# Optimization experiments

Measured on AMD Instinct MI355X. Metric: run time of the kernel, lower is better.

## Reference

```python
import jax, jax.numpy as jnp
import numpy as np

H = 32          # hidden_size
L = 10          # linear_size
EPS = 1e-14


def _lstm_cell(x, h, c, Wih, Whh, bih, bhh):
    # torch LSTMCell: gates ordered [i, f, g, o]
    gates = x @ Wih.T + bih + h @ Whh.T + bhh
    i, f, g, o = jnp.split(gates, 4, axis=-1)
    i = jax.nn.sigmoid(i)
    f = jax.nn.sigmoid(f)
    g = jnp.tanh(g)
    o = jax.nn.sigmoid(o)
    c_new = f * c + i * g
    h_new = o * jnp.tanh(c_new)
    return h_new, c_new


def setup_inputs() -> dict:
    key = jax.random.key(0)
    ks = jax.random.split(key, 24)
    B, N = 8, 100000
    inp = {
        "x": jax.random.normal(ks[0], (B, N), jnp.float32),
        "grad": jax.random.normal(ks[1], (B, N), jnp.float32),
        "h0": jax.random.normal(ks[2], (B, N, H), jnp.float32),
        "c0": jax.random.normal(ks[3], (B, N, H), jnp.float32),
        "h1": jax.random.normal(ks[4], (B, N, H), jnp.float32),
        "c1": jax.random.normal(ks[5], (B, N, H), jnp.float32),
        # initial_transform: Linear(2, L) -> tanh -> Linear(L, L)
        "W1": jax.random.normal(ks[6], (L, 2), jnp.float32) * 0.3,
        "b1": jax.random.normal(ks[7], (L,), jnp.float32) * 0.1,
        "W2": jax.random.normal(ks[8], (L, L), jnp.float32) * 0.3,
        "b2": jax.random.normal(ks[9], (L,), jnp.float32) * 0.1,
        # LSTMCell layer 0 (input L) and layer 1 (input H)
        "Wih0": jax.random.normal(ks[10], (4 * H, L), jnp.float32) * 0.1,
        "Whh0": jax.random.normal(ks[11], (4 * H, H), jnp.float32) * 0.1,
        "bih0": jax.random.normal(ks[12], (4 * H,), jnp.float32) * 0.1,
        "bhh0": jax.random.normal(ks[13], (4 * H,), jnp.float32) * 0.1,
        "Wih1": jax.random.normal(ks[14], (4 * H, H), jnp.float32) * 0.1,
        "Whh1": jax.random.normal(ks[15], (4 * H, H), jnp.float32) * 0.1,
        "bih1": jax.random.normal(ks[16], (4 * H,), jnp.float32) * 0.1,
        "bhh1": jax.random.normal(ks[17], (4 * H,), jnp.float32) * 0.1,
        # fc: Linear(H, 1)
        "Wfc": jax.random.normal(ks[18], (1, H), jnp.float32) * 0.1,
        "bfc": jax.random.normal(ks[19], (1,), jnp.float32) * 0.1,
    }
    return inp


def reference(x, grad, h0, c0, h1, c1, W1, b1, W2, b2,
              Wih0, Whh0, bih0, bhh0, Wih1, Whh1, bih1, bhh1, Wfc, bfc):
    B, N = x.shape
    BN = B * N
    g = grad.reshape(BN, 1)
    # gradient preprocessing: [sign, log(|g| + eps)]
    inp = jnp.concatenate([jnp.sign(g), jnp.log(jnp.abs(g) + EPS)], axis=1)  # (BN, 2)
    t = jnp.tanh(inp @ W1.T + b1) @ W2.T + b2                                # (BN, L)
    # batched across all n variables simultaneously (no cross-variable recurrence)
    h0n, c0n = _lstm_cell(t, h0.reshape(BN, H), c0.reshape(BN, H), Wih0, Whh0, bih0, bhh0)
    h1n, c1n = _lstm_cell(h0n, h1.reshape(BN, H), c1.reshape(BN, H), Wih1, Whh1, bih1, bhh1)
    delta = (h1n @ Wfc.T + bfc).reshape(B, N)
    x_new = x + delta
    return (x_new,
            h0n.reshape(B, N, H), c0n.reshape(B, N, H),
            h1n.reshape(B, N, H), c1n.reshape(B, N, H),
            delta)
```

## Files before the change

kernel.cpp:

```cpp
#include <hip/hip_runtime.h>


typedef __attribute__((ext_vector_type(8))) short bf16x8;
typedef __attribute__((ext_vector_type(4))) float f32x4;

#define HH 32
#define LL 10
#define NG 128
#define NW 8
#define BLK 512
#define TP 36

__device__ __forceinline__ short f2bf(float x) {
  __bf16 b = (__bf16)x;
  return __builtin_bit_cast(short, b);
}
__device__ __forceinline__ float fsig(float x) {
  return __builtin_amdgcn_rcpf(1.0f + __expf(-x));
}
__device__ __forceinline__ float ftanh(float x) {
  return fmaf(2.0f, __builtin_amdgcn_rcpf(1.0f + __expf(-2.0f * x)), -1.0f);
}
#define LDS_FENCE() asm volatile("s_waitcnt lgkmcnt(0)" ::: "memory")

#define LOADT(P, STV) do {                                                   \
    const size_t ro_ = (size_t)(ebase + (STV) * 16 + col) * HH + 8 * g;      \
    P##hv0 = reinterpret_cast<const float4*>(h0 + ro_)[0];                   \
    P##hv1 = reinterpret_cast<const float4*>(h0 + ro_)[1];                   \
    P##cv0 = reinterpret_cast<const float4*>(c0 + ro_)[0];                   \
    P##cv1 = reinterpret_cast<const float4*>(c0 + ro_)[1];                   \
    P##wv0 = reinterpret_cast<const float4*>(h1 + ro_)[0];                   \
    P##wv1 = reinterpret_cast<const float4*>(h1 + ro_)[1];                   \
    P##dv0 = reinterpret_cast<const float4*>(c1 + ro_)[0];                   \
    P##dv1 = reinterpret_cast<const float4*>(c1 + ro_)[1];                   \
  } while (0)

#define COMPUTE(P, STV) do {                                                  \
    const int m16_ = ebase + (STV) * 16;                                      \
    const size_t rowoff_ = (size_t)(m16_ + col) * HH + 8 * g;                 \
    bf16x8 a_t = {0, 0, 0, 0, 0, 0, 0, 0};                                    \
    if (g == 0) a_t = *reinterpret_cast<const bf16x8*>(&tsg0[w][(STV) * 16 + col][0]); \
    else if (g == 1) {                                                        \
      a_t[0] = tsg1[w][(STV) * 16 + col][0];                                  \
      a_t[1] = tsg1[w][(STV) * 16 + col][1];                                  \
    }                                                                         \
    bf16x8 a_h0;                                                              \
    a_h0[0] = f2bf(P##hv0.x); a_h0[1] = f2bf(P##hv0.y);                       \
    a_h0[2] = f2bf(P##hv0.z); a_h0[3] = f2bf(P##hv0.w);                       \
    a_h0[4] = f2bf(P##hv1.x); a_h0[5] = f2bf(P##hv1.y);                       \
    a_h0[6] = f2bf(P##hv1.z); a_h0[7] = f2bf(P##hv1.w);                       \
    f32x4 acc[8];                                                             \
    _Pragma("unroll")                                                         \
    for (int nt = 0; nt < 8; ++nt) {                                          \
      float bv = biasv0[nt];                                                  \
      f32x4 a = {bv, bv, bv, bv};                                             \
      acc[nt] = a;                                                            \
    }                                                                         \
    _Pragma("unroll")                                                         \
    for (int nt = 0; nt < 8; ++nt) {                                          \
      bf16x8 bih = {0, 0, 0, 0, 0, 0, 0, 0};                                  \
      if (g < 2) bih = *reinterpret_cast<const bf16x8*>(&wih0L[g][nt * 16 + col][0]); \
      acc[nt] = __builtin_amdgcn_mfma_f32_16x16x32_bf16(a_t, bih, acc[nt], 0, 0, 0);  \
      bf16x8 bhh = *reinterpret_cast<const bf16x8*>(&whh0L[g][nt * 16 + col][0]);     \
      acc[nt] = __builtin_amdgcn_mfma_f32_16x16x32_bf16(a_h0, bhh, acc[nt], 0, 0, 0); \
    }                                                                         \
    *reinterpret_cast<float4*>(&tbuf[w][col][8 * g])     = P##cv0;            \
    *reinterpret_cast<float4*>(&tbuf[w][col][8 * g + 4]) = P##cv1;            \
    LDS_FENCE();                                                              \
    float c0r[2][4];                                                          \
    _Pragma("unroll")                                                         \
    for (int kk = 0; kk < 2; ++kk)                                            \
      _Pragma("unroll")                                                       \
      for (int r = 0; r < 4; ++r)                                             \
        c0r[kk][r] = tbuf[w][mrow + r][16 * kk + col];                        \
    LDS_FENCE();                                                              \
    float hnv[2][4], cnv[2][4];                                               \
    _Pragma("unroll")                                                         \
    for (int kk = 0; kk < 2; ++kk)                                            \
      _Pragma("unroll")                                                       \
      for (int r = 0; r < 4; ++r) {                                           \
        float iv = fsig(acc[0 + kk][r]);                                      \
        float fv = fsig(acc[2 + kk][r]);                                      \
        float gv = ftanh(acc[4 + kk][r]);                                     \
        float ov = fsig(acc[6 + kk][r]);                                      \
        float cn = fv * c0r[kk][r] + iv * gv;                                 \
        float hn = ov * ftanh(cn);                                            \
        cnv[kk][r] = cn;                                                      \
        hnv[kk][r] = hn;                                                      \
      }                                                                       \
    _Pragma("unroll")                                                         \
    for (int kk = 0; kk < 2; ++kk)                                            \
      _Pragma("unroll")                                                       \
      for (int r = 0; r < 4; ++r)                                             \
        tbuf[w][mrow + r][16 * kk + col] = hnv[kk][r];                        \
    LDS_FENCE();                                                              \
    float4 hnr0 = *reinterpret_cast<const float4*>(&tbuf[w][col][8 * g]);     \
    float4 hnr1 = *reinterpret_cast<const float4*>(&tbuf[w][col][8 * g + 4]); \
    LDS_FENCE();                                                              \
    *reinterpret_cast<float4*>(h0out + rowoff_)     = hnr0;                   \
    *reinterpret_cast<float4*>(h0out + rowoff_ + 4) = hnr1;                   \
    bf16x8 a_hn;                                                              \
    a_hn[0] = f2bf(hnr0.x); a_hn[1] = f2bf(hnr0.y);                           \
    a_hn[2] = f2bf(hnr0.z); a_hn[3] = f2bf(hnr0.w);                           \
    a_hn[4] = f2bf(hnr1.x); a_hn[5] = f2bf(hnr1.y);                           \
    a_hn[6] = f2bf(hnr1.z); a_hn[7] = f2bf(hnr1.w);                           \
    _Pragma("unroll")                                                         \
    for (int kk = 0; kk < 2; ++kk)                                            \
      _Pragma("unroll")                                                       \
      for (int r = 0; r < 4; ++r)                                             \
        tbuf[w][mrow + r][16 * kk + col] = cnv[kk][r];                        \
    LDS_FENCE();                                                              \
    float4 cnr0 = *reinterpret_cast<const float4*>(&tbuf[w][col][8 * g]);     \
    float4 cnr1 = *reinterpret_cast<const float4*>(&tbuf[w][col][8 * g + 4]); \
    LDS_FENCE();                                                              \
    *reinterpret_cast<float4*>(c0out + rowoff_)     = cnr0;                   \
    *reinterpret_cast<float4*>(c0out + rowoff_ + 4) = cnr1;                   \
    *reinterpret_cast<float4*>(&tbuf[w][col][8 * g])     = P##dv0;            \
    *reinterpret_cast<float4*>(&tbuf[w][col][8 * g + 4]) = P##dv1;            \
    LDS_FENCE();                                                              \
    float c1r[2][4];                                                          \
    _Pragma("unroll")                                                         \
    for (int kk = 0; kk < 2; ++kk)                                            \
      _Pragma("unroll")                                                       \
      for (int r = 0; r < 4; ++r)                                             \
        c1r[kk][r] = tbuf[w][mrow + r][16 * kk + col];                        \
    LDS_FENCE();                                                              \
    bf16x8 a_h1;                                                              \
    a_h1[0] = f2bf(P##wv0.x); a_h1[1] = f2bf(P##wv0.y);                       \
    a_h1[2] = f2bf(P##wv0.z); a_h1[3] = f2bf(P##wv0.w);                       \
    a_h1[4] = f2bf(P##wv1.x); a_h1[5] = f2bf(P##wv1.y);                       \
    a_h1[6] = f2bf(P##wv1.z); a_h1[7] = f2bf(P##wv1.w);                       \
    _Pragma("unroll")                                                         \
    for (int nt = 0; nt < 8; ++nt) {                                          \
      float bv = biasv1[nt];                                                  \
      f32x4 a = {bv, bv, bv, bv};                                             \
      acc[nt] = a;                                                            \
    }                                                                         \
    _Pragma("unroll")                                                         \
    for (int nt = 0; nt < 8; ++nt) {                                          \
      bf16x8 bih = *reinterpret_cast<const bf16x8*>(&wih1L[g][nt * 16 + col][0]);     \
      acc[nt] = __builtin_amdgcn_mfma_f32_16x16x32_bf16(a_hn, bih, acc[nt], 0, 0, 0); \
      bf16x8 bhh = *reinterpret_cast<const bf16x8*>(&whh1L[g][nt * 16 + col][0]);     \
      acc[nt] = __builtin_amdgcn_mfma_f32_16x16x32_bf16(a_h1, bhh, acc[nt], 0, 0, 0); \
    }                                                                         \
    float dsum[4] = {0.f, 0.f, 0.f, 0.f};                                     \
    _Pragma("unroll")                                                         \
    for (int kk = 0; kk < 2; ++kk) {                                          \
      const float wf = kk ? wfc1 : wfc0;                                      \
      _Pragma("unroll")                                                       \
      for (int r = 0; r < 4; ++r) {                                           \
        float iv = fsig(acc[0 + kk][r]);                                      \
        float fv = fsig(acc[2 + kk][r]);                                      \
        float gv = ftanh(acc[4 + kk][r]);                                     \
        float ov = fsig(acc[6 + kk][r]);                                      \
        float cn = fv * c1r[kk][r] + iv * gv;                                 \
        float hn = ov * ftanh(cn);                                            \
        cnv[kk][r] = cn;                                                      \
        hnv[kk][r] = hn;                                                      \
        dsum[r] += hn * wf;                                                   \
      }                                                                       \
    }                                                                         \
    _Pragma("unroll")                                                         \
    for (int kk = 0; kk < 2; ++kk)                                            \
      _Pragma("unroll")                                                       \
      for (int r = 0; r < 4; ++r)                                             \
        tbuf[w][mrow + r][16 * kk + col] = hnv[kk][r];                        \
    LDS_FENCE();                                                              \
    float4 h1r0 = *reinterpret_cast<const float4*>(&tbuf[w][col][8 * g]);     \
    float4 h1r1 = *reinterpret_cast<const float4*>(&tbuf[w][col][8 * g + 4]); \
    LDS_FENCE();                                                              \
    *reinterpret_cast<float4*>(h1out + rowoff_)     = h1r0;                   \
    *reinterpret_cast<float4*>(h1out + rowoff_ + 4) = h1r1;                   \
    _Pragma("unroll")                                                         \
    for (int kk = 0; kk < 2; ++kk)                                            \
      _Pragma("unroll")                                                       \
      for (int r = 0; r < 4; ++r)                                             \
        tbuf[w][mrow + r][16 * kk + col] = cnv[kk][r];                        \
    LDS_FENCE();                                                              \
    float4 c1r0 = *reinterpret_cast<const float4*>(&tbuf[w][col][8 * g]);     \
    float4 c1r1 = *reinterpret_cast<const float4*>(&tbuf[w][col][8 * g + 4]); \
    LDS_FENCE();                                                              \
    *reinterpret_cast<float4*>(c1out + rowoff_)     = c1r0;                   \
    *reinterpret_cast<float4*>(c1out + rowoff_ + 4) = c1r1;                   \
    _Pragma("unroll")                                                         \
    for (int off = 1; off < 16; off <<= 1) {                                  \
      _Pragma("unroll")                                                       \
      for (int r = 0; r < 4; ++r) dsum[r] += __shfl_xor(dsum[r], off, 64);    \
    }                                                                         \
    if (col == 0) {                                                           \
      const int e4 = m16_ + mrow;                                             \
      float4 xv = *reinterpret_cast<const float4*>(x + e4);                   \
      float4 dv = {dsum[0] + bfcv, dsum[1] + bfcv, dsum[2] + bfcv, dsum[3] + bfcv}; \
      *reinterpret_cast<float4*>(dout + e4) = dv;                             \
      float4 xn = {xv.x + dv.x, xv.y + dv.y, xv.z + dv.z, xv.w + dv.w};       \
      *reinterpret_cast<float4*>(xout + e4) = xn;                             \
    }                                                                         \
  } while (0)

__global__ __launch_bounds__(BLK, 2) void l2o_fused(
    const float* __restrict__ x, const float* __restrict__ grad,
    const float* __restrict__ h0, const float* __restrict__ c0,
    const float* __restrict__ h1, const float* __restrict__ c1,
    const float* __restrict__ W1, const float* __restrict__ b1,
    const float* __restrict__ W2, const float* __restrict__ b2,
    const float* __restrict__ Wih0, const float* __restrict__ Whh0,
    const float* __restrict__ bih0, const float* __restrict__ bhh0,
    const float* __restrict__ Wih1, const float* __restrict__ Whh1,
    const float* __restrict__ bih1, const float* __restrict__ bhh1,
    const float* __restrict__ Wfc, const float* __restrict__ bfc,
    float* __restrict__ out, int BNi)
{
  const size_t BN = (size_t)BNi;
  float* __restrict__ xout  = out;
  float* __restrict__ h0out = out + BN;
  float* __restrict__ c0out = out + BN + BN * HH;
  float* __restrict__ h1out = out + BN + 2 * BN * HH;
  float* __restrict__ c1out = out + BN + 3 * BN * HH;
  float* __restrict__ dout  = out + BN + 4 * BN * HH;

  __shared__ __align__(16) short wih0L[2][NG][8];
  __shared__ __align__(16) short whh0L[4][NG][8];
  __shared__ __align__(16) short wih1L[4][NG][8];
  __shared__ __align__(16) short whh1L[4][NG][8];
  __shared__ __align__(16) short tsg0[NW][64][8];
  __shared__ __align__(4)  short tsg1[NW][64][2];
  __shared__ __align__(16) float tbuf[NW][16][TP];

  const int tid = threadIdx.x;
  const int lane = tid & 63;
  const int w = tid >> 6;
  const int col = lane & 15;
  const int g = lane >> 4;
  const int mrow = 4 * g;

  const int ebase = blockIdx.x * (NW * 64) + w * 64;
  const bool active = ebase < BNi;

  float4 Ahv0, Ahv1, Acv0, Acv1, Awv0, Awv1, Adv0, Adv1;
  float4 Bhv0, Bhv1, Bcv0, Bcv1, Bwv0, Bwv1, Bdv0, Bdv1;

  if (active) LOADT(A, 0);

  for (int idx = tid; idx < NG * HH; idx += BLK) {
    int n = idx >> 5, k = idx & 31;
    whh0L[k >> 3][n][k & 7] = f2bf(Whh0[n * HH + k]);
    wih1L[k >> 3][n][k & 7] = f2bf(Wih1[n * HH + k]);
    whh1L[k >> 3][n][k & 7] = f2bf(Whh1[n * HH + k]);
  }
  for (int idx = tid; idx < NG * 16; idx += BLK) {
    int n = idx >> 4, k = idx & 15;
    wih0L[k >> 3][n][k & 7] = (k < LL) ? f2bf(Wih0[n * LL + k]) : (short)0;
  }

  float biasv0[8], biasv1[8];
#pragma unroll
  for (int nt = 0; nt < 8; ++nt) {
    biasv0[nt] = bih0[nt * 16 + col] + bhh0[nt * 16 + col];
    biasv1[nt] = bih1[nt * 16 + col] + bhh1[nt * 16 + col];
  }
  const float wfc0 = Wfc[col], wfc1 = Wfc[16 + col];
  const float bfcv = bfc[0];

  if (active) {
    float gv = grad[ebase + lane];
    float sg = (gv > 0.f) ? 1.f : ((gv < 0.f) ? -1.f : 0.f);
    float lg = __logf(fabsf(gv) + 1e-14f);
    float u[LL], t[LL];
#pragma unroll
    for (int j = 0; j < LL; ++j)
      u[j] = ftanh(W1[2 * j] * sg + W1[2 * j + 1] * lg + b1[j]);
#pragma unroll
    for (int j = 0; j < LL; ++j) {
      float a = b2[j];
#pragma unroll
      for (int k = 0; k < LL; ++k) a += W2[j * LL + k] * u[k];
      t[j] = a;
    }
    bf16x8 tv0;
#pragma unroll
    for (int s = 0; s < 8; ++s) tv0[s] = f2bf(t[s]);
    *reinterpret_cast<bf16x8*>(&tsg0[w][lane][0]) = tv0;
    tsg1[w][lane][0] = f2bf(t[8]);
    tsg1[w][lane][1] = f2bf(t[9]);
  }
  __syncthreads();

  if (active) {
    LOADT(B, 1);
    COMPUTE(A, 0);
    LOADT(A, 2);
    COMPUTE(B, 1);
    LOADT(B, 3);
    COMPUTE(A, 2);
    COMPUTE(B, 3);
  }
}

extern "C" void kernel_launch(void* const* d_in, const int* in_sizes, int n_in,
                              void* d_out, int out_size, void* d_ws, size_t ws_size,
                              hipStream_t stream) {
  const float* x    = (const float*)d_in[0];
  const float* grad = (const float*)d_in[1];
  const float* h0   = (const float*)d_in[2];
  const float* c0   = (const float*)d_in[3];
  const float* h1   = (const float*)d_in[4];
  const float* c1   = (const float*)d_in[5];
  const float* W1   = (const float*)d_in[6];
  const float* b1   = (const float*)d_in[7];
  const float* W2   = (const float*)d_in[8];
  const float* b2   = (const float*)d_in[9];
  const float* Wih0 = (const float*)d_in[10];
  const float* Whh0 = (const float*)d_in[11];
  const float* bih0 = (const float*)d_in[12];
  const float* bhh0 = (const float*)d_in[13];
  const float* Wih1 = (const float*)d_in[14];
  const float* Whh1 = (const float*)d_in[15];
  const float* bih1 = (const float*)d_in[16];
  const float* bhh1 = (const float*)d_in[17];
  const float* Wfc  = (const float*)d_in[18];
  const float* bfc  = (const float*)d_in[19];
  const int BN = in_sizes[0];
  const int nblk = (BN + BLK - 1) / BLK;
  l2o_fused<<<nblk, BLK, 0, stream>>>(x, grad, h0, c0, h1, c1, W1, b1, W2, b2,
                                      Wih0, Whh0, bih0, bhh0, Wih1, Whh1,
                                      bih1, bhh1, Wfc, bfc, (float*)d_out, BN);
}
```

Baseline: 208.8 us.

## Swap MFMA operand roles so gate outputs land row-major, dropping LDS transposes

Result: no change. 208.4 us (-0.2%).

```diff
diff --git a/kernel.cpp b/kernel.cpp
--- a/kernel.cpp
+++ b/kernel.cpp
@@ -2,6 +2,7 @@
 
 
 typedef __attribute__((ext_vector_type(8))) short bf16x8;
+typedef __attribute__((ext_vector_type(4))) short bf16x4;
 typedef __attribute__((ext_vector_type(4))) float f32x4;
 
 #define HH 32
@@ -9,7 +10,7 @@
 #define NG 128
 #define NW 8
 #define BLK 512
-#define TP 36
+#define TPS 36
 
 __device__ __forceinline__ short f2bf(float x) {
   __bf16 b = (__bf16)x;
@@ -23,177 +24,123 @@
 }
 #define LDS_FENCE() asm volatile("s_waitcnt lgkmcnt(0)" ::: "memory")
 
-#define LOADT(P, STV) do {                                                   \
-    const size_t ro_ = (size_t)(ebase + (STV) * 16 + col) * HH + 8 * g;      \
-    P##hv0 = reinterpret_cast<const float4*>(h0 + ro_)[0];                   \
-    P##hv1 = reinterpret_cast<const float4*>(h0 + ro_)[1];                   \
-    P##cv0 = reinterpret_cast<const float4*>(c0 + ro_)[0];                   \
-    P##cv1 = reinterpret_cast<const float4*>(c0 + ro_)[1];                   \
-    P##wv0 = reinterpret_cast<const float4*>(h1 + ro_)[0];                   \
-    P##wv1 = reinterpret_cast<const float4*>(h1 + ro_)[1];                   \
-    P##dv0 = reinterpret_cast<const float4*>(c1 + ro_)[0];                   \
-    P##dv1 = reinterpret_cast<const float4*>(c1 + ro_)[1];                   \
+#define LOADH(P, STV) do {                                                    \
+    const size_t ro_ = (size_t)(ebase + (STV) * 16 + col) * HH + 8 * g;       \
+    P##hv0 = reinterpret_cast<const float4*>(h0 + ro_)[0];                    \
+    P##hv1 = reinterpret_cast<const float4*>(h0 + ro_)[1];                    \
+    P##wv0 = reinterpret_cast<const float4*>(h1 + ro_)[0];                    \
+    P##wv1 = reinterpret_cast<const float4*>(h1 + ro_)[1];                    \
   } while (0)
 
 #define COMPUTE(P, STV) do {                                                  \
     const int m16_ = ebase + (STV) * 16;                                      \
-    const size_t rowoff_ = (size_t)(m16_ + col) * HH + 8 * g;                 \
-    bf16x8 a_t = {0, 0, 0, 0, 0, 0, 0, 0};                                    \
-    if (g == 0) a_t = *reinterpret_cast<const bf16x8*>(&tsg0[w][(STV) * 16 + col][0]); \
-    else if (g == 1) {                                                        \
-      a_t[0] = tsg1[w][(STV) * 16 + col][0];                                  \
-      a_t[1] = tsg1[w][(STV) * 16 + col][1];                                  \
-    }                                                                         \
-    bf16x8 a_h0;                                                              \
-    a_h0[0] = f2bf(P##hv0.x); a_h0[1] = f2bf(P##hv0.y);                       \
-    a_h0[2] = f2bf(P##hv0.z); a_h0[3] = f2bf(P##hv0.w);                       \
-    a_h0[4] = f2bf(P##hv1.x); a_h0[5] = f2bf(P##hv1.y);                       \
-    a_h0[6] = f2bf(P##hv1.z); a_h0[7] = f2bf(P##hv1.w);                       \
+    const size_t ro_ = (size_t)(m16_ + col) * HH;                             \
+    \
+    float4 cv0 = *reinterpret_cast<const float4*>(c0 + ro_ + 4 * g);          \
+    float4 cv1 = *reinterpret_cast<const float4*>(c0 + ro_ + 16 + 4 * g);     \
+    float4 dv0 = *reinterpret_cast<const float4*>(c1 + ro_ + 4 * g);          \
+    float4 dv1 = *reinterpret_cast<const float4*>(c1 + ro_ + 16 + 4 * g);     \
+                                                     \
+    bf16x8 b_t = {0, 0, 0, 0, 0, 0, 0, 0};                                    \
+    if (g < 2) b_t = *reinterpret_cast<const bf16x8*>(&tsg[w][(STV) * 16 + col][8 * g]); \
+    bf16x8 b_h0;                                                              \
+    b_h0[0] = f2bf(P##hv0.x); b_h0[1] = f2bf(P##hv0.y);                       \
+    b_h0[2] = f2bf(P##hv0.z); b_h0[3] = f2bf(P##hv0.w);                       \
+    b_h0[4] = f2bf(P##hv1.x); b_h0[5] = f2bf(P##hv1.y);                       \
+    b_h0[6] = f2bf(P##hv1.z); b_h0[7] = f2bf(P##hv1.w);                       \
     f32x4 acc[8];                                                             \
     _Pragma("unroll")                                                         \
+    for (int nt = 0; nt < 8; ++nt) { f32x4 z = {0.f, 0.f, 0.f, 0.f}; acc[nt] = z; } \
+    _Pragma("unroll")                                                         \
     for (int nt = 0; nt < 8; ++nt) {                                          \
-      float bv = biasv0[nt];                                                  \
-      f32x4 a = {bv, bv, bv, bv};                                             \
-      acc[nt] = a;                                                            \
-    }                                                                         \
-    _Pragma("unroll")                                                         \
-    for (int nt = 0; nt < 8; ++nt) {                                          \
-      bf16x8 bih = {0, 0, 0, 0, 0, 0, 0, 0};                                  \
-      if (g < 2) bih = *reinterpret_cast<const bf16x8*>(&wih0L[g][nt * 16 + col][0]); \
-      acc[nt] = __builtin_amdgcn_mfma_f32_16x16x32_bf16(a_t, bih, acc[nt], 0, 0, 0);  \
-      bf16x8 bhh = *reinterpret_cast<const bf16x8*>(&whh0L[g][nt * 16 + col][0]);     \
-      acc[nt] = __builtin_amdgcn_mfma_f32_16x16x32_bf16(a_h0, bhh, acc[nt], 0, 0, 0); \
-    }                                                                         \
-    *reinterpret_cast<float4*>(&tbuf[w][col][8 * g])     = P##cv0;            \
-    *reinterpret_cast<float4*>(&tbuf[w][col][8 * g + 4]) = P##cv1;            \
-    LDS_FENCE();                                                              \
-    float c0r[2][4];                                                          \
-    _Pragma("unroll")                                                         \
-    for (int kk = 0; kk < 2; ++kk)                                            \
-      _Pragma("unroll")                                                       \
-      for (int r = 0; r < 4; ++r)                                             \
-        c0r[kk][r] = tbuf[w][mrow + r][16 * kk + col];                        \
-    LDS_FENCE();                                                              \
+      bf16x8 a_ih = *reinterpret_cast<const bf16x8*>(&wih0L[g & 1][nt * 16 + col][0]); \
+      acc[nt] = __builtin_amdgcn_mfma_f32_16x16x32_bf16(a_ih, b_t, acc[nt], 0, 0, 0);  \
+      bf16x8 a_hh = *reinterpret_cast<const bf16x8*>(&whh0L[g][nt * 16 + col][0]);     \
+      acc[nt] = __builtin_amdgcn_mfma_f32_16x16x32_bf16(a_hh, b_h0, acc[nt], 0, 0, 0); \
+    }                                                                         \
+                   \
     float hnv[2][4], cnv[2][4];                                               \
     _Pragma("unroll")                                                         \
     for (int kk = 0; kk < 2; ++kk)                                            \
       _Pragma("unroll")                                                       \
       for (int r = 0; r < 4; ++r) {                                           \
-        float iv = fsig(acc[0 + kk][r]);                                      \
+        float iv = fsig(acc[kk][r]);                                          \
         float fv = fsig(acc[2 + kk][r]);                                      \
         float gv = ftanh(acc[4 + kk][r]);                                     \
         float ov = fsig(acc[6 + kk][r]);                                      \
-        float cn = fv * c0r[kk][r] + iv * gv;                                 \
-        float hn = ov * ftanh(cn);                                            \
+        float cp = kk ? cv1[r] : cv0[r];                                      \
+        float cn = fv * cp + iv * gv;                                         \
         cnv[kk][r] = cn;                                                      \
-        hnv[kk][r] = hn;                                                      \
+        hnv[kk][r] = ov * ftanh(cn);                                          \
       }                                                                       \
+    {                                \
+      float4 s0 = {cnv[0][0], cnv[0][1], cnv[0][2], cnv[0][3]};               \
+      float4 s1 = {cnv[1][0], cnv[1][1], cnv[1][2], cnv[1][3]};               \
+      *reinterpret_cast<float4*>(c0out + ro_ + 4 * g)      = s0;              \
+      *reinterpret_cast<float4*>(c0out + ro_ + 16 + 4 * g) = s1;              \
+      float4 t0 = {hnv[0][0], hnv[0][1], hnv[0][2], hnv[0][3]};               \
+      float4 t1 = {hnv[1][0], hnv[1][1], hnv[1][2], hnv[1][3]};               \
+      *reinterpret_cast<float4*>(h0out + ro_ + 4 * g)      = t0;              \
+      *reinterpret_cast<float4*>(h0out + ro_ + 16 + 4 * g) = t1;              \
+    }                                                                         \
+     \
+    {                                                                         \
+      bf16x4 p0 = {f2bf(hnv[0][0]), f2bf(hnv[0][1]), f2bf(hnv[0][2]), f2bf(hnv[0][3])}; \
+      bf16x4 p1 = {f2bf(hnv[1][0]), f2bf(hnv[1][1]), f2bf(hnv[1][2]), f2bf(hnv[1][3])}; \
+      *reinterpret_cast<bf16x4*>(&tbuf[w][col][4 * g])      = p0;             \
+      *reinterpret_cast<bf16x4*>(&tbuf[w][col][16 + 4 * g]) = p1;             \
+    }                                                                         \
+    LDS_FENCE();                                                              \
+    bf16x8 b_hn = *reinterpret_cast<const bf16x8*>(&tbuf[w][col][8 * g]);     \
+    LDS_FENCE();           \
+    bf16x8 b_h1;                                                              \
+    b_h1[0] = f2bf(P##wv0.x); b_h1[1] = f2bf(P##wv0.y);                       \
+    b_h1[2] = f2bf(P##wv0.z); b_h1[3] = f2bf(P##wv0.w);                       \
+    b_h1[4] = f2bf(P##wv1.x); b_h1[5] = f2bf(P##wv1.y);                       \
+    b_h1[6] = f2bf(P##wv1.z); b_h1[7] = f2bf(P##wv1.w);                       \
+    _Pragma("unroll")                                                         \
+    for (int nt = 0; nt < 8; ++nt) acc[nt] = biasv1[nt];                      \
+    _Pragma("unroll")                                                         \
+    for (int nt = 0; nt < 8; ++nt) {                                          \
+      bf16x8 a_ih = *reinterpret_cast<const bf16x8*>(&wih1L[g][nt * 16 + col][0]);     \
+      acc[nt] = __builtin_amdgcn_mfma_f32_16x16x32_bf16(a_ih, b_hn, acc[nt], 0, 0, 0); \
+      bf16x8 a_hh = *reinterpret_cast<const bf16x8*>(&whh1L[g][nt * 16 + col][0]);     \
+      acc[nt] = __builtin_amdgcn_mfma_f32_16x16x32_bf16(a_hh, b_h1, acc[nt], 0, 0, 0); \
+    }                                                                         \
     _Pragma("unroll")                                                         \
     for (int kk = 0; kk < 2; ++kk)                                            \
       _Pragma("unroll")                                                       \
-      for (int r = 0; r < 4; ++r)                                             \
-        tbuf[w][mrow + r][16 * kk + col] = hnv[kk][r];                        \
-    LDS_FENCE();                                                              \
-    float4 hnr0 = *reinterpret_cast<const float4*>(&tbuf[w][col][8 * g]);     \
-    float4 hnr1 = *reinterpret_cast<const float4*>(&tbuf[w][col][8 * g + 4]); \
-    LDS_FENCE();                                                              \
-    *reinterpret_cast<float4*>(h0out + rowoff_)     = hnr0;                   \
-    *reinterpret_cast<float4*>(h0out + rowoff_ + 4) = hnr1;                   \
-    bf16x8 a_hn;                                                              \
-    a_hn[0] = f2bf(hnr0.x); a_hn[1] = f2bf(hnr0.y);                           \
-    a_hn[2] = f2bf(hnr0.z); a_hn[3] = f2bf(hnr0.w);                           \
-    a_hn[4] = f2bf(hnr1.x); a_hn[5] = f2bf(hnr1.y);                           \
-    a_hn[6] = f2bf(hnr1.z); a_hn[7] = f2bf(hnr1.w);                           \
-    _Pragma("unroll")                                                         \
-    for (int kk = 0; kk < 2; ++kk)                                            \
-      _Pragma("unroll")                                                       \
-      for (int r = 0; r < 4; ++r)                                             \
-        tbuf[w][mrow + r][16 * kk + col] = cnv[kk][r];                        \
-    LDS_FENCE();                                                              \
-    float4 cnr0 = *reinterpret_cast<const float4*>(&tbuf[w][col][8 * g]);     \
-    float4 cnr1 = *reinterpret_cast<const float4*>(&tbuf[w][col][8 * g + 4]); \
-    LDS_FENCE();                                                              \
-    *reinterpret_cast<float4*>(c0out + rowoff_)     = cnr0;                   \
-    *reinterpret_cast<float4*>(c0out + rowoff_ + 4) = cnr1;                   \
-    *reinterpret_cast<float4*>(&tbuf[w][col][8 * g])     = P##dv0;            \
-    *reinterpret_cast<float4*>(&tbuf[w][col][8 * g + 4]) = P##dv1;            \
-    LDS_FENCE();                                                              \
-    float c1r[2][4];                                                          \
-    _Pragma("unroll")                                                         \
-    for (int kk = 0; kk < 2; ++kk)                                            \
-      _Pragma("unroll")                                                       \
-      for (int r = 0; r < 4; ++r)                                             \
-        c1r[kk][r] = tbuf[w][mrow + r][16 * kk + col];                        \
-    LDS_FENCE();                                                              \
-    bf16x8 a_h1;                                                              \
-    a_h1[0] = f2bf(P##wv0.x); a_h1[1] = f2bf(P##wv0.y);                       \
-    a_h1[2] = f2bf(P##wv0.z); a_h1[3] = f2bf(P##wv0.w);                       \
-    a_h1[4] = f2bf(P##wv1.x); a_h1[5] = f2bf(P##wv1.y);                       \
-    a_h1[6] = f2bf(P##wv1.z); a_h1[7] = f2bf(P##wv1.w);                       \
-    _Pragma("unroll")                                                         \
-    for (int nt = 0; nt < 8; ++nt) {                                          \
-      float bv = biasv1[nt];                                                  \
-      f32x4 a = {bv, bv, bv, bv};                                             \
-      acc[nt] = a;                                                            \
-    }                                                                         \
-    _Pragma("unroll")                                                         \
-    for (int nt = 0; nt < 8; ++nt) {                                          \
-      bf16x8 bih = *reinterpret_cast<const bf16x8*>(&wih1L[g][nt * 16 + col][0]);     \
-      acc[nt] = __builtin_amdgcn_mfma_f32_16x16x32_bf16(a_hn, bih, acc[nt], 0, 0, 0); \
-      bf16x8 bhh = *reinterpret_cast<const bf16x8*>(&whh1L[g][nt * 16 + col][0]);     \
-      acc[nt] = __builtin_amdgcn_mfma_f32_16x16x32_bf16(a_h1, bhh, acc[nt], 0, 0, 0); \
-    }                                                                         \
-    float dsum[4] = {0.f, 0.f, 0.f, 0.f};                                     \
-    _Pragma("unroll")                                                         \
-    for (int kk = 0; kk < 2; ++kk) {                                          \
-      const float wf = kk ? wfc1 : wfc0;                                      \
-      _Pragma("unroll")                                                       \
       for (int r = 0; r < 4; ++r) {                                           \
-        float iv = fsig(acc[0 + kk][r]);                                      \
+        float iv = fsig(acc[kk][r]);                                          \
         float fv = fsig(acc[2 + kk][r]);                                      \
         float gv = ftanh(acc[4 + kk][r]);                                     \
         float ov = fsig(acc[6 + kk][r]);                                      \
-        float cn = fv * c1r[kk][r] + iv * gv;                                 \
-        float hn = ov * ftanh(cn);                                            \
+        float cp = kk ? dv1[r] : dv0[r];                                      \
+        float cn = fv * cp + iv * gv;                                         \
         cnv[kk][r] = cn;                                                      \
-        hnv[kk][r] = hn;                                                      \
-        dsum[r] += hn * wf;                                                   \
+        hnv[kk][r] = ov * ftanh(cn);                                          \
       }                                                                       \
-    }                                                                         \
-    _Pragma("unroll")                                                         \
-    for (int kk = 0; kk < 2; ++kk)                                            \
-      _Pragma("unroll")                                                       \
-      for (int r = 0; r < 4; ++r)                                             \
-        tbuf[w][mrow + r][16 * kk + col] = hnv[kk][r];                        \
-    LDS_FENCE();                                                              \
-    float4 h1r0 = *reinterpret_cast<const float4*>(&tbuf[w][col][8 * g]);     \
-    float4 h1r1 = *reinterpret_cast<const float4*>(&tbuf[w][col][8 * g + 4]); \
-    LDS_FENCE();                                                              \
-    *reinterpret_cast<float4*>(h1out + rowoff_)     = h1r0;                   \
-    *reinterpret_cast<float4*>(h1out + rowoff_ + 4) = h1r1;                   \
-    _Pragma("unroll")                                                         \
-    for (int kk = 0; kk < 2; ++kk)                                            \
-      _Pragma("unroll")                                                       \
-      for (int r = 0; r < 4; ++r)                                             \
-        tbuf[w][mrow + r][16 * kk + col] = cnv[kk][r];                        \
-    LDS_FENCE();                                                              \
-    float4 c1r0 = *reinterpret_cast<const float4*>(&tbuf[w][col][8 * g]);     \
-    float4 c1r1 = *reinterpret_cast<const float4*>(&tbuf[w][col][8 * g + 4]); \
-    LDS_FENCE();                                                              \
-    *reinterpret_cast<float4*>(c1out + rowoff_)     = c1r0;                   \
-    *reinterpret_cast<float4*>(c1out + rowoff_ + 4) = c1r1;                   \
-    _Pragma("unroll")                                                         \
-    for (int off = 1; off < 16; off <<= 1) {                                  \
-      _Pragma("unroll")                                                       \
-      for (int r = 0; r < 4; ++r) dsum[r] += __shfl_xor(dsum[r], off, 64);    \
-    }                                                                         \
-    if (col == 0) {                                                           \
-      const int e4 = m16_ + mrow;                                             \
-      float4 xv = *reinterpret_cast<const float4*>(x + e4);                   \
-      float4 dv = {dsum[0] + bfcv, dsum[1] + bfcv, dsum[2] + bfcv, dsum[3] + bfcv}; \
-      *reinterpret_cast<float4*>(dout + e4) = dv;                             \
-      float4 xn = {xv.x + dv.x, xv.y + dv.y, xv.z + dv.z, xv.w + dv.w};       \
-      *reinterpret_cast<float4*>(xout + e4) = xn;                             \
+    {                                                                         \
+      float4 s0 = {cnv[0][0], cnv[0][1], cnv[0][2], cnv[0][3]};               \
+      float4 s1 = {cnv[1][0], cnv[1][1], cnv[1][2], cnv[1][3]};               \
+      *reinterpret_cast<float4*>(c1out + ro_ + 4 * g)      = s0;              \
+      *reinterpret_cast<float4*>(c1out + ro_ + 16 + 4 * g) = s1;              \
+      float4 t0 = {hnv[0][0], hnv[0][1], hnv[0][2], hnv[0][3]};               \
+      float4 t1 = {hnv[1][0], hnv[1][1], hnv[1][2], hnv[1][3]};               \
+      *reinterpret_cast<float4*>(h1out + ro_ + 4 * g)      = t0;              \
+      *reinterpret_cast<float4*>(h1out + ro_ + 16 + 4 * g) = t1;              \
+    }                                                                         \
+    float dsum = 0.f;                                                         \
+    _Pragma("unroll")                                                         \
+    for (int r = 0; r < 4; ++r)                                               \
+      dsum += hnv[0][r] * wfcA[r] + hnv[1][r] * wfcB[r];                      \
+    dsum += __shfl_xor(dsum, 16, 64);                                         \
+    dsum += __shfl_xor(dsum, 32, 64);                                         \
+    if (g == 0) {                                                             \
+      float xv = x[m16_ + col];                                               \
+      float dv = dsum + bfcv;                                                 \
+      dout[m16_ + col] = dv;                                                  \
+      xout[m16_ + col] = xv + dv;                                             \
     }                                                                         \
   } while (0)
 
@@ -222,24 +169,21 @@
   __shared__ __align__(16) short whh0L[4][NG][8];
   __shared__ __align__(16) short wih1L[4][NG][8];
   __shared__ __align__(16) short whh1L[4][NG][8];
-  __shared__ __align__(16) short tsg0[NW][64][8];
-  __shared__ __align__(4)  short tsg1[NW][64][2];
-  __shared__ __align__(16) float tbuf[NW][16][TP];
+  __shared__ __align__(16) short tsg[NW][64][16];
+  __shared__ __align__(16) short tbuf[NW][16][TPS];
 
   const int tid = threadIdx.x;
   const int lane = tid & 63;
   const int w = tid >> 6;
   const int col = lane & 15;
   const int g = lane >> 4;
-  const int mrow = 4 * g;
 
   const int ebase = blockIdx.x * (NW * 64) + w * 64;
   const bool active = ebase < BNi;
 
-  float4 Ahv0, Ahv1, Acv0, Acv1, Awv0, Awv1, Adv0, Adv1;
-  float4 Bhv0, Bhv1, Bcv0, Bcv1, Bwv0, Bwv1, Bdv0, Bdv1;
-
-  if (active) LOADT(A, 0);
+  float4 Ahv0, Ahv1, Awv0, Awv1;
+  float4 Bhv0, Bhv1, Bwv0, Bwv1;
+  if (active) LOADH(A, 0);
 
   for (int idx = tid; idx < NG * HH; idx += BLK) {
     int n = idx >> 5, k = idx & 31;
@@ -249,16 +193,23 @@
   }
   for (int idx = tid; idx < NG * 16; idx += BLK) {
     int n = idx >> 4, k = idx & 15;
-    wih0L[k >> 3][n][k & 7] = (k < LL) ? f2bf(Wih0[n * LL + k]) : (short)0;
-  }
-
-  float biasv0[8], biasv1[8];
+    short v;
+    if (k < LL)       v = f2bf(Wih0[n * LL + k]);
+    else if (k == LL) v = f2bf(bih0[n] + bhh0[n]);
+    else              v = 0;
+    wih0L[k >> 3][n][k & 7] = v;
+  }
+
+  f32x4 biasv1[8];
 #pragma unroll
   for (int nt = 0; nt < 8; ++nt) {
-    biasv0[nt] = bih0[nt * 16 + col] + bhh0[nt * 16 + col];
-    biasv1[nt] = bih1[nt * 16 + col] + bhh1[nt * 16 + col];
-  }
-  const float wfc0 = Wfc[col], wfc1 = Wfc[16 + col];
+    float4 a = *reinterpret_cast<const float4*>(bih1 + nt * 16 + 4 * g);
+    float4 b = *reinterpret_cast<const float4*>(bhh1 + nt * 16 + 4 * g);
+    f32x4 s = {a.x + b.x, a.y + b.y, a.z + b.z, a.w + b.w};
+    biasv1[nt] = s;
+  }
+  float4 wfcA = *reinterpret_cast<const float4*>(Wfc + 4 * g);
+  float4 wfcB = *reinterpret_cast<const float4*>(Wfc + 16 + 4 * g);
   const float bfcv = bfc[0];
 
   if (active) {
@@ -276,21 +227,24 @@
       for (int k = 0; k < LL; ++k) a += W2[j * LL + k] * u[k];
       t[j] = a;
     }
-    bf16x8 tv0;
+    bf16x8 tv0, tv1;
 #pragma unroll
     for (int s = 0; s < 8; ++s) tv0[s] = f2bf(t[s]);
-    *reinterpret_cast<bf16x8*>(&tsg0[w][lane][0]) = tv0;
-    tsg1[w][lane][0] = f2bf(t[8]);
-    tsg1[w][lane][1] = f2bf(t[9]);
+    tv1[0] = f2bf(t[8]); tv1[1] = f2bf(t[9]);
+    tv1[2] = 0x3F80;
+#pragma unroll
+    for (int s = 3; s < 8; ++s) tv1[s] = 0;
+    *reinterpret_cast<bf16x8*>(&tsg[w][lane][0]) = tv0;
+    *reinterpret_cast<bf16x8*>(&tsg[w][lane][8]) = tv1;
   }
   __syncthreads();
 
   if (active) {
-    LOADT(B, 1);
+    LOADH(B, 1);
     COMPUTE(A, 0);
-    LOADT(A, 2);
+    LOADH(A, 2);
     COMPUTE(B, 1);
-    LOADT(B, 3);
+    LOADH(B, 3);
     COMPUTE(A, 2);
     COMPUTE(B, 3);
   }
```
